# Optimization experiments

Measured on AMD Instinct MI355X. Metric: run time of the kernel, lower is better.

The kernel has to match this reference:

```python
import jax, jax.numpy as jnp
import numpy as np

B, CIN, COUT, K, LDIM, HW = 16, 512, 512, 3, 512, 32


def setup_inputs() -> dict:
    key = jax.random.key(0)
    ks = jax.random.split(key, 4)
    return {
        "x": jax.random.normal(ks[0], (B, CIN, HW, HW), jnp.float32),
        "w": jax.random.normal(ks[1], (B, LDIM), jnp.float32),
        "mod_w": jax.random.normal(ks[2], (CIN, LDIM), jnp.float32) * 0.02,
        "mod_b": jnp.zeros((CIN,), jnp.float32),
        "ln_g": jnp.ones((CIN,), jnp.float32),
        "ln_b": jnp.zeros((CIN,), jnp.float32),
        "weight": jax.random.normal(ks[3], (COUT, CIN, K, K), jnp.float32) * 0.02,
        "scale": jnp.ones((1, CIN, 1, 1), jnp.float32),
    }


def reference(x, w, mod_w, mod_b, ln_g, ln_b, weight, scale):
    eps = 1e-8
    b, cin, H, W = x.shape
    cout, _, k, _ = weight.shape
    # modulation MLP: Linear -> LayerNorm -> LeakyReLU(0.2)
    s = w @ mod_w.T + mod_b                                   # [b, cin]
    mu = s.mean(-1, keepdims=True)
    var = s.var(-1, keepdims=True)
    s = (s - mu) * jax.lax.rsqrt(var + 1e-5) * ln_g + ln_b
    s = jnp.where(s >= 0, s, 0.2 * s)
    # modulate per-sample weights: [b, cout, cin, k, k]
    s = s.reshape(b, 1, cin, 1, 1) * scale.reshape(1, 1, cin, 1, 1)
    wmod = weight[None] * s
    # demodulate
    d = jax.lax.rsqrt(jnp.sum(wmod * wmod, axis=(2, 3, 4)) + eps)  # [b, cout]
    wmod = wmod * d.reshape(b, cout, 1, 1, 1)
    # batch-as-groups conv2d
    wg = wmod.reshape(b * cout, cin, k, k)
    xg = x.reshape(1, b * cin, H, W)
    pad = k // 2
    out = jax.lax.conv_general_dilated(
        xg, wg, window_strides=(1, 1), padding=[(pad, pad), (pad, pad)],
        dimension_numbers=("NCHW", "OIHW", "NCHW"), feature_group_count=b)
    return out.reshape(b, cout, H, W)
```

## Files before the change

kernel.cpp:

```cpp
#include <hip/hip_runtime.h>

typedef unsigned short u16;
typedef __bf16 bf16x8 __attribute__((ext_vector_type(8)));
typedef float  f32x16 __attribute__((ext_vector_type(16)));

__device__ __forceinline__ u16 f2bf(float f) {
    union { float f; unsigned u; } v; v.f = f;
    return (u16)((v.u + 0x7fffu + ((v.u >> 16) & 1u)) >> 16);
}

#define GLD16(gsrc, ldst) \
    __builtin_amdgcn_global_load_lds( \
        (const __attribute__((address_space(1))) void*)(gsrc), \
        (__attribute__((address_space(3))) void*)(ldst), 16, 0, 0)

__global__ __launch_bounds__(256) void lin_kernel(
    const float* __restrict__ w, const float* __restrict__ mod_w,
    const float* __restrict__ mod_b, float* __restrict__ s_raw)
{
    int gw = (blockIdx.x * 256 + threadIdx.x) >> 6;
    int lane = threadIdx.x & 63;
    int b = gw >> 9, c = gw & 511;
    const float* wr = w + b * 512;
    const float* mr = mod_w + (size_t)c * 512;
    float a = 0.f;
#pragma unroll
    for (int i = 0; i < 8; ++i)
        a = fmaf(wr[lane + i * 64], mr[lane + i * 64], a);
    for (int off = 32; off; off >>= 1) a += __shfl_down(a, off);
    if (!lane) s_raw[gw] = a + mod_b[c];
}

__global__ __launch_bounds__(512) void norm_kernel(
    const float* __restrict__ s_raw, const float* __restrict__ ln_g,
    const float* __restrict__ ln_b, const float* __restrict__ scale,
    float* __restrict__ s_eff)
{
    int b = blockIdx.x, c = threadIdx.x;
    __shared__ float rs[512], rq[512];
    float s = s_raw[b * 512 + c];
    rs[c] = s; rq[c] = s * s;
    __syncthreads();
    for (int off = 256; off; off >>= 1) {
        if (c < off) { rs[c] += rs[c + off]; rq[c] += rq[c + off]; }
        __syncthreads();
    }
    float mean = rs[0] * (1.f / 512.f);
    float var  = rq[0] * (1.f / 512.f) - mean * mean;
    float sn = (s - mean) * rsqrtf(var + 1e-5f) * ln_g[c] + ln_b[c];
    sn = sn >= 0.f ? sn : 0.2f * sn;
    s_eff[b * 512 + c] = sn * scale[c];
}

__global__ __launch_bounds__(256) void wsq_kernel(
    const float* __restrict__ weight, float* __restrict__ wsq, u16* __restrict__ wbfT)
{
    int idx = blockIdx.x * 256 + threadIdx.x;
    int co = idx >> 9, ci = idx & 511;
    int cg = ci >> 3, cj = ci & 7;
    const float* wp = weight + (size_t)idx * 9;
    float s = 0.f;
#pragma unroll
    for (int p = 0; p < 9; ++p) {
        float v = wp[p];
        s += v * v;
        wbfT[((size_t)(p * 64 + cg) * 512 + co) * 8 + cj] = f2bf(v);
    }
    wsq[idx] = s;
}

__global__ __launch_bounds__(256) void xs_kernel(
    const float* __restrict__ x, const float* __restrict__ s_eff,
    u16* __restrict__ xs)
{
    const int bh = blockIdx.x;
    const int b = bh >> 5, h = bh & 31;
    __shared__ float tile[64][33];
    for (int c0 = 0; c0 < 512; c0 += 64) {
        if (c0) __syncthreads();
        for (int idx = threadIdx.x; idx < 2048; idx += 256) {
            int c = idx >> 5, ww = idx & 31;
            tile[c][ww] = x[(((size_t)b * 512 + c0 + c) * 32 + h) * 32 + ww]
                          * s_eff[b * 512 + c0 + c];
        }
        __syncthreads();
        for (int idx = threadIdx.x; idx < 2048; idx += 256) {
            int ww = idx >> 6, c = idx & 63;
            xs[((b * 32 + h) * 32 + ww) * 512 + c0 + c] = f2bf(tile[c][ww]);
        }
    }
}

__global__ __launch_bounds__(256) void dsc_kernel(
    const float* __restrict__ s_eff, const float* __restrict__ wsq,
    float* __restrict__ dsc)
{
    int gw = (blockIdx.x * 256 + threadIdx.x) >> 6;
    int lane = threadIdx.x & 63;
    int b = gw >> 9, co = gw & 511;
    float a = 0.f;
#pragma unroll
    for (int i = 0; i < 8; ++i) {
        int cin = lane + i * 64;
        float se = s_eff[b * 512 + cin];
        a += se * se * wsq[co * 512 + cin];
    }
    for (int off = 32; off; off >>= 1) a += __shfl_down(a, off);
    if (!lane) dsc[gw] = rsqrtf(a + 1e-8f);
}

__global__ void zfill_kernel(float* p) { p[threadIdx.x] = 0.f; }

__global__ __launch_bounds__(512) void conv_kernel(
    const u16* __restrict__ wbfT,
    const u16* __restrict__ xs,
    const float* __restrict__ dsc,
    const u16* __restrict__ zp,
    float* __restrict__ out)
{
    __shared__ __align__(16) u16 lds[2 * 816 * 8];

    const int tid  = threadIdx.x;
    const int lane = tid & 63;
    const int wv   = tid >> 6;
    const int wm   = wv >> 1;
    const int wn   = wv & 1;
    const int l31  = lane & 31;
    const int kc8  = lane >> 5;

    const int bx = blockIdx.x;
    const int mt = bx & 1;
    const int nt = bx >> 1;
    const int b  = nt >> 3;
    const int h0 = (nt & 7) << 2;

    const u16* xsb = xs + (size_t)b * (32 * 32 * 512);

    const u16* sb[4]; bool sval[4], inb[4];
#pragma unroll
    for (int k = 0; k < 4; ++k) {
        int ch = tid + k * 512;
        sval[k] = ch < 816;
        int p = ch >> 2, slot = ch & 3;
        int kc = slot ^ ((p >> 1) & 3);
        int rr = p / 34, cc = p % 34;
        int hh = h0 - 1 + rr, ww = cc - 1;
        inb[k] = sval[k] && ((unsigned)hh < 32u) && ((unsigned)ww < 32u);
        sb[k] = xsb + (hh * 32 + ww) * 512 + kc * 8;
    }
    char* ldsb = (char*)lds;
    char* wdst = ldsb + wv * 1024;

    auto stage = [&](int buf, int c0) {
        char* d = wdst + buf * 13056;
#pragma unroll
        for (int k = 0; k < 2; ++k)
            if (sval[k]) GLD16(inb[k] ? sb[k] + c0 : zp, d + k * 8192);
    };

    const u16* apb[2];
#pragma unroll
    for (int mf = 0; mf < 2; ++mf)
        apb[mf] = wbfT + ((size_t)kc8 * 512 + mt * 256 + wm * 64 + mf * 32 + l31) * 8;

    uint4 aA[2][2], aB[2][2];
    auto loadA = [&](uint4 (&dst)[2][2], int pos, int c0g) {
#pragma unroll
        for (int mf = 0; mf < 2; ++mf)
#pragma unroll
            for (int kk = 0; kk < 2; ++kk)
                dst[mf][kk] = *reinterpret_cast<const uint4*>(
                    apb[mf] + ((size_t)(pos * 64 + c0g) + kk * 2) * 4096);
    };

    f32x16 acc[2][2] = {};

    stage(0, 0);
    loadA(aA, 0, 0);
    __syncthreads();

    for (int r = 0; r < 16; ++r) {
        const int c0g = r * 4;
        const char* base = ldsb + (r & 1) * 13056;
        if (r < 15) stage((r + 1) & 1, (r + 1) * 32);

#pragma unroll
        for (int pos = 0; pos < 9; ++pos) {
            const int kh = pos / 3, kw = pos % 3;
            if (pos < 8) {
                if ((pos & 1) == 0) loadA(aB, pos + 1, c0g);
                else                loadA(aA, pos + 1, c0g);
            } else if (r < 15) {
                loadA(aB, 0, c0g + 4);
            }
#pragma unroll
            for (int kk = 0; kk < 2; ++kk) {
                const int sk = kk * 2 + kc8;
                bf16x8 bv[2];
#pragma unroll
                for (int nf = 0; nf < 2; ++nf) {
                    const int p = (wn * 2 + nf + kh) * 34 + l31 + kw;
                    bv[nf] = *reinterpret_cast<const bf16x8*>(
                        base + p * 64 + ((sk ^ ((p >> 1) & 3)) << 4));
                }
                const uint4* af = ((pos & 1) == 0) ? &aA[0][0] : &aB[0][0];
#pragma unroll
                for (int mf = 0; mf < 2; ++mf) {
                    bf16x8 av = *reinterpret_cast<const bf16x8*>(&af[mf * 2 + kk]);
                    acc[mf][0] = __builtin_amdgcn_mfma_f32_32x32x16_bf16(
                        av, bv[0], acc[mf][0], 0, 0, 0);
                    acc[mf][1] = __builtin_amdgcn_mfma_f32_32x32x16_bf16(
                        av, bv[1], acc[mf][1], 0, 0, 0);
                }
            }
        }
        if (r < 15) {
#pragma unroll
            for (int mf = 0; mf < 2; ++mf)
#pragma unroll
                for (int kk = 0; kk < 2; ++kk) aA[mf][kk] = aB[mf][kk];
        }
        __syncthreads();
    }

    const float* db = dsc + b * 512;
#pragma unroll
    for (int mf = 0; mf < 2; ++mf) {
#pragma unroll
        for (int nf = 0; nf < 2; ++nf) {
            const int px = wn * 64 + nf * 32 + l31;
            const int h = h0 + (px >> 5), w = px & 31;
#pragma unroll
            for (int q = 0; q < 16; ++q) {
                int row = (q & 3) + 8 * (q >> 2) + 4 * kc8;
                int co  = mt * 256 + wm * 64 + mf * 32 + row;
                out[(((size_t)b * 512 + co) * 32 + h) * 32 + w]
                    = acc[mf][nf][q] * db[co];
            }
        }
    }
}

extern "C" void kernel_launch(void* const* d_in, const int* in_sizes, int n_in,
                              void* d_out, int out_size, void* d_ws, size_t ws_size,
                              hipStream_t stream) {
    const float* x      = (const float*)d_in[0];
    const float* w      = (const float*)d_in[1];
    const float* mod_w  = (const float*)d_in[2];
    const float* mod_b  = (const float*)d_in[3];
    const float* ln_g   = (const float*)d_in[4];
    const float* ln_b   = (const float*)d_in[5];
    const float* weight = (const float*)d_in[6];
    const float* scale  = (const float*)d_in[7];
    float* out = (float*)d_out;

    char* ws = (char*)d_ws;
    float* s_raw = (float*)(ws);
    float* dsc   = (float*)(ws);
    float* s_eff = (float*)(ws + 32768);
    float* wsq   = (float*)(ws + 65536);
    u16*   wbfT  = (u16*)(ws + 65536 + 1048576);
    u16*   xs    = (u16*)(ws + 65536 + 1048576 + 4718592);
    if (ws_size < 22609920u) return;

    lin_kernel <<<2048, 256, 0, stream>>>(w, mod_w, mod_b, s_raw);
    wsq_kernel <<<1024, 256, 0, stream>>>(weight, wsq, wbfT);
    norm_kernel<<<16, 512, 0, stream>>>(s_raw, ln_g, ln_b, scale, s_eff);
    xs_kernel  <<<512, 256, 0, stream>>>(x, s_eff, xs);
    dsc_kernel <<<2048, 256, 0, stream>>>(s_eff, wsq, dsc);
    zfill_kernel<<<1, 1024, 0, stream>>>(s_eff);
    conv_kernel<<<256, 512, 0, stream>>>(wbfT, xs, dsc, (const u16*)s_eff, out);
}
```

Measured before the change: 137.0 us.

## Stage conv weights through LDS with triple-buffered async pipeline and explicit waitcnts

```diff
diff --git a/kernel.cpp b/kernel.cpp
--- a/kernel.cpp
+++ b/kernel.cpp
@@ -118,7 +118,8 @@
     const u16* __restrict__ zp,
     float* __restrict__ out)
 {
-    __shared__ __align__(16) u16 lds[2 * 816 * 8];
+    __shared__ __align__(16) u16 ldsA[3 * 8192];
+    __shared__ __align__(16) u16 ldsB[2 * 8192];
 
     const int tid  = threadIdx.x;
     const int lane = tid & 63;
@@ -135,92 +136,111 @@
     const int h0 = (nt & 7) << 2;
 
     const u16* xsb = xs + (size_t)b * (32 * 32 * 512);
-
-    const u16* sb[4]; bool sval[4], inb[4];
-#pragma unroll
-    for (int k = 0; k < 4; ++k) {
+    char* ldsAc = (char*)ldsA;
+    char* ldsBc = (char*)ldsB;
+
+    const u16* asrc0; const u16* asrc1;
+    {
+        int co0 = tid >> 2,        kc0 = (tid & 3) ^ ((co0 >> 1) & 3);
+        int co1 = (tid + 512) >> 2, kc1 = ((tid + 512) & 3) ^ ((co1 >> 1) & 3);
+        asrc0 = wbfT + ((size_t)kc0 * 512 + mt * 256 + co0) * 8;
+        asrc1 = wbfT + ((size_t)kc1 * 512 + mt * 256 + co1) * 8;
+    }
+    auto issueA = [&](int pos_st, int cg_st, int buf) {
+        size_t off = (size_t)(pos_st * 64 + cg_st * 4) * 4096;
+        char* d = ldsAc + buf * 16384 + wv * 1024;
+        GLD16(asrc0 + off, d);
+        GLD16(asrc1 + off, d + 8192);
+    };
+
+    const u16* bsrc[2]; bool binb[2];
+#pragma unroll
+    for (int k = 0; k < 2; ++k) {
         int ch = tid + k * 512;
-        sval[k] = ch < 816;
         int p = ch >> 2, slot = ch & 3;
         int kc = slot ^ ((p >> 1) & 3);
         int rr = p / 34, cc = p % 34;
         int hh = h0 - 1 + rr, ww = cc - 1;
-        inb[k] = sval[k] && ((unsigned)hh < 32u) && ((unsigned)ww < 32u);
-        sb[k] = xsb + (hh * 32 + ww) * 512 + kc * 8;
-    }
-    char* ldsb = (char*)lds;
-    char* wdst = ldsb + wv * 1024;
-
-    auto stage = [&](int buf, int c0) {
-        char* d = wdst + buf * 13056;
-#pragma unroll
-        for (int k = 0; k < 2; ++k)
-            if (sval[k]) GLD16(inb[k] ? sb[k] + c0 : zp, d + k * 8192);
+        binb[k] = (ch < 816) && ((unsigned)hh < 32u) && ((unsigned)ww < 32u);
+        bsrc[k] = xsb + (hh * 32 + ww) * 512 + kc * 8;
+    }
+    auto issueB = [&](int buf, int c0) {
+        char* d = ldsBc + buf * 16384 + wv * 1024;
+        GLD16(binb[0] ? bsrc[0] + c0 : zp, d);
+        GLD16(binb[1] ? bsrc[1] + c0 : zp, d + 8192);
     };
 
-    const u16* apb[2];
-#pragma unroll
-    for (int mf = 0; mf < 2; ++mf)
-        apb[mf] = wbfT + ((size_t)kc8 * 512 + mt * 256 + wm * 64 + mf * 32 + l31) * 8;
-
-    uint4 aA[2][2], aB[2][2];
-    auto loadA = [&](uint4 (&dst)[2][2], int pos, int c0g) {
-#pragma unroll
-        for (int mf = 0; mf < 2; ++mf)
+    const int aswz = (l31 >> 1) & 3;
+    f32x16 acc[2][2] = {};
+
+    issueA(0, 0, 0);
+    issueB(0, 0);
+    issueA(1, 0, 1);
+    asm volatile("s_waitcnt vmcnt(2)" ::: "memory");
+    __builtin_amdgcn_s_barrier();
+
+    for (int r = 0; r < 16; ++r) {
+        const char* bb = ldsBc + (r & 1) * 16384;
+        const bool last = (r == 15);
+
+#pragma unroll
+        for (int s = 0; s < 9; ++s) {
+            const int kh = s / 3, kw = s % 3;
+            const char* ab = ldsAc + (s % 3) * 16384;
+
+            bf16x8 af[2][2], bfv[2][2];
+#pragma unroll
+            for (int mf = 0; mf < 2; ++mf)
+#pragma unroll
+                for (int kk = 0; kk < 2; ++kk) {
+                    int co = wm * 64 + mf * 32 + l31;
+                    int ph = (kk * 2 + kc8) ^ aswz;
+                    af[mf][kk] = *reinterpret_cast<const bf16x8*>(
+                        ab + co * 64 + ph * 16);
+                }
 #pragma unroll
             for (int kk = 0; kk < 2; ++kk)
-                dst[mf][kk] = *reinterpret_cast<const uint4*>(
-                    apb[mf] + ((size_t)(pos * 64 + c0g) + kk * 2) * 4096);
-    };
-
-    f32x16 acc[2][2] = {};
-
-    stage(0, 0);
-    loadA(aA, 0, 0);
-    __syncthreads();
-
-    for (int r = 0; r < 16; ++r) {
-        const int c0g = r * 4;
-        const char* base = ldsb + (r & 1) * 13056;
-        if (r < 15) stage((r + 1) & 1, (r + 1) * 32);
-
-#pragma unroll
-        for (int pos = 0; pos < 9; ++pos) {
-            const int kh = pos / 3, kw = pos % 3;
-            if (pos < 8) {
-                if ((pos & 1) == 0) loadA(aB, pos + 1, c0g);
-                else                loadA(aA, pos + 1, c0g);
-            } else if (r < 15) {
-                loadA(aB, 0, c0g + 4);
+#pragma unroll
+                for (int nf = 0; nf < 2; ++nf) {
+                    int p = (wn * 2 + nf + kh) * 34 + l31 + kw;
+                    int ph = (kk * 2 + kc8) ^ ((p >> 1) & 3);
+                    bfv[kk][nf] = *reinterpret_cast<const bf16x8*>(
+                        bb + p * 64 + ph * 16);
+                }
+
+            if (s <= 6)      issueA(s + 2, r, (s + 2) % 3);
+            else if (!last)  issueA(s - 7, r + 1, (s + 2) % 3);
+            if (s == 4 && !last) issueB((r + 1) & 1, (r + 1) * 32);
+
+            __builtin_amdgcn_s_barrier();
+            asm volatile("s_waitcnt lgkmcnt(0)" ::: "memory");
+            __builtin_amdgcn_sched_barrier(0);
+
+            __builtin_amdgcn_s_setprio(1);
+#pragma unroll
+            for (int kk = 0; kk < 2; ++kk) {
+                acc[0][0] = __builtin_amdgcn_mfma_f32_32x32x16_bf16(af[0][kk], bfv[kk][0], acc[0][0], 0, 0, 0);
+                acc[0][1] = __builtin_amdgcn_mfma_f32_32x32x16_bf16(af[0][kk], bfv[kk][1], acc[0][1], 0, 0, 0);
+                acc[1][0] = __builtin_amdgcn_mfma_f32_32x32x16_bf16(af[1][kk], bfv[kk][0], acc[1][0], 0, 0, 0);
+                acc[1][1] = __builtin_amdgcn_mfma_f32_32x32x16_bf16(af[1][kk], bfv[kk][1], acc[1][1], 0, 0, 0);
             }
-#pragma unroll
-            for (int kk = 0; kk < 2; ++kk) {
-                const int sk = kk * 2 + kc8;
-                bf16x8 bv[2];
-#pragma unroll
-                for (int nf = 0; nf < 2; ++nf) {
-                    const int p = (wn * 2 + nf + kh) * 34 + l31 + kw;
-                    bv[nf] = *reinterpret_cast<const bf16x8*>(
-                        base + p * 64 + ((sk ^ ((p >> 1) & 3)) << 4));
-                }
-                const uint4* af = ((pos & 1) == 0) ? &aA[0][0] : &aB[0][0];
-#pragma unroll
-                for (int mf = 0; mf < 2; ++mf) {
-                    bf16x8 av = *reinterpret_cast<const bf16x8*>(&af[mf * 2 + kk]);
-                    acc[mf][0] = __builtin_amdgcn_mfma_f32_32x32x16_bf16(
-                        av, bv[0], acc[mf][0], 0, 0, 0);
-                    acc[mf][1] = __builtin_amdgcn_mfma_f32_32x32x16_bf16(
-                        av, bv[1], acc[mf][1], 0, 0, 0);
+            __builtin_amdgcn_s_setprio(0);
+            __builtin_amdgcn_sched_barrier(0);
+
+            if (!last) {
+                if (s == 4 || s == 5) asm volatile("s_waitcnt vmcnt(4)" ::: "memory");
+                else                  asm volatile("s_waitcnt vmcnt(2)" ::: "memory");
+                __builtin_amdgcn_s_barrier();
+            } else {
+                if (s <= 6) {
+                    asm volatile("s_waitcnt vmcnt(2)" ::: "memory");
+                    __builtin_amdgcn_s_barrier();
+                } else if (s == 7) {
+                    asm volatile("s_waitcnt vmcnt(0)" ::: "memory");
+                    __builtin_amdgcn_s_barrier();
                 }
             }
         }
-        if (r < 15) {
-#pragma unroll
-            for (int mf = 0; mf < 2; ++mf)
-#pragma unroll
-                for (int kk = 0; kk < 2; ++kk) aA[mf][kk] = aB[mf][kk];
-        }
-        __syncthreads();
     }
 
     const float* db = dsc + b * 512;
```

Result: slower. 149.0 us (+8.8%).
